# Kernel optimization log

Measured on AMD Instinct MI355X. Metric: run time of the kernel, lower is better.

Reference implementation:

```python
import jax, jax.numpy as jnp
import numpy as np

BN_EPS = 1e-5
RES_SCALE = 0.7


def setup_inputs() -> dict:
    key = jax.random.key(0)
    ks = jax.random.split(key, 10)
    N, IN_DIM, HID, E, L = 50000, 2000, 64, 1600000, 4
    features = jax.random.normal(ks[0], (N, IN_DIM), dtype=jnp.float32)
    edges = jax.random.randint(ks[1], (2, E), 0, N, dtype=jnp.int64)
    # GCNConv params: layer 0 is in_dim->hid, layers 1..3 are hid->hid
    W0 = jax.random.normal(ks[2], (IN_DIM, HID), dtype=jnp.float32) / np.sqrt(IN_DIM)
    b0 = jnp.zeros((HID,), dtype=jnp.float32)
    Wh = jax.random.normal(ks[3], (L - 1, HID, HID), dtype=jnp.float32) / np.sqrt(HID)
    bh = jnp.zeros((L - 1, HID), dtype=jnp.float32)
    # BatchNorm1d affine params per layer
    gamma = jnp.ones((L, HID), dtype=jnp.float32)
    beta = jnp.zeros((L, HID), dtype=jnp.float32)
    # learned layer-mixing weights (torch.randn init)
    lw = jax.random.normal(ks[4], (L,), dtype=jnp.float32)
    return {"features": features, "edges": edges, "W0": W0, "b0": b0,
            "Wh": Wh, "bh": bh, "gamma": gamma, "beta": beta, "lw": lw}


def reference(features, edges, W0, b0, Wh, bh, gamma, beta, lw):
    n = features.shape[0]
    src, dst = edges[0], edges[1]
    # GCN symmetric normalization with self-loops, edge_weight=1
    deg = jnp.zeros((n,), features.dtype).at[dst].add(1.0) + 1.0  # +1 self loop
    dinv = jax.lax.rsqrt(deg)
    enorm = dinv[src] * dinv[dst]       # [E]
    snorm = dinv * dinv                 # [N], self-loop norm

    def gcn_conv(x, W, b):
        xw = x @ W                                            # [N, H]
        agg = jnp.zeros_like(xw).at[dst].add(xw[src] * enorm[:, None])
        agg = agg + xw * snorm[:, None]
        return agg + b

    def batchnorm(x, g, bt):
        m = x.mean(axis=0)
        v = x.var(axis=0)  # biased variance, as in BN training normalization
        return (x - m) * jax.lax.rsqrt(v + BN_EPS) * g + bt

    L = gamma.shape[0]
    Ws = [W0] + [Wh[i] for i in range(L - 1)]
    bs = [b0] + [bh[i] for i in range(L - 1)]

    layer_out = []
    x = features
    for i in range(L):
        x = gcn_conv(x, Ws[i], bs[i])
        x = jax.nn.relu(batchnorm(x, gamma[i], beta[i]))
        if i > 0:
            x = x + RES_SCALE * layer_out[i - 1]
        layer_out.append(x)

    w = jax.nn.softmax(lw)
    emb = layer_out[0] * w[0]
    for i in range(1, L):
        emb = emb + layer_out[i] * w[i]
    return emb
```

## Files before the change

### kernel.cpp

```cpp
#include <hip/hip_runtime.h>
#include <hip/hip_bf16.h>
#include <math.h>

#define BN_EPS 1e-5f
#define RES_SCALE 0.7f

typedef float f4 __attribute__((ext_vector_type(4)));
typedef short s8 __attribute__((ext_vector_type(8)));

__device__ inline short f2bf(float f) {
    __hip_bfloat16 h = __float2bfloat16(f);
    return *reinterpret_cast<short*>(&h);
}

__global__ __launch_bounds__(256) void k_zero(int* counts, int* cursor, float* stats, int N, int S) {
    int i = blockIdx.x * 256 + threadIdx.x;
    if (i < N) { counts[i] = 0; cursor[i] = 0; }
    if (i < S) stats[i] = 0.0f;
}

__global__ __launch_bounds__(256) void k_count(const int* __restrict__ edges, int E, int* __restrict__ counts) {
    int e = blockIdx.x * 256 + threadIdx.x;
    if (e < E) atomicAdd(&counts[edges[E + e]], 1);
}

__global__ __launch_bounds__(256) void k_dinv(const int* __restrict__ counts, float* __restrict__ dinv, int N) {
    int i = blockIdx.x * 256 + threadIdx.x;
    if (i < N) dinv[i] = rsqrtf((float)counts[i] + 1.0f);
}

__global__ __launch_bounds__(256) void k_scan1(const int* __restrict__ counts, int* __restrict__ bsum, int N) {
    __shared__ int sd[256];
    int t = threadIdx.x;
    int base = blockIdx.x * 1024 + t * 4;
    int s = 0;
    if (base + 3 < N) { int4 v = *(const int4*)(counts + base); s = v.x + v.y + v.z + v.w; }
    else { for (int j = 0; j < 4; ++j) if (base + j < N) s += counts[base + j]; }
    sd[t] = s; __syncthreads();
    for (int off = 128; off > 0; off >>= 1) { if (t < off) sd[t] += sd[t + off]; __syncthreads(); }
    if (t == 0) bsum[blockIdx.x] = sd[0];
}

__global__ void k_scan2(int* bsum, int B, int* rowstart, int N) {
    if (threadIdx.x == 0 && blockIdx.x == 0) {
        int run = 0;
        for (int b = 0; b < B; ++b) { int v = bsum[b]; bsum[b] = run; run += v; }
        rowstart[N] = run;
    }
}

__global__ __launch_bounds__(256) void k_scan3(const int* __restrict__ counts, const int* __restrict__ bsum,
                                               int* __restrict__ rowstart, int N) {
    __shared__ int sd[256];
    int t = threadIdx.x;
    int base = blockIdx.x * 1024 + t * 4;
    int v0 = 0, v1 = 0, v2 = 0, v3 = 0;
    if (base + 3 < N) { int4 v = *(const int4*)(counts + base); v0 = v.x; v1 = v.y; v2 = v.z; v3 = v.w; }
    else {
        if (base < N) v0 = counts[base];
        if (base + 1 < N) v1 = counts[base + 1];
        if (base + 2 < N) v2 = counts[base + 2];
        if (base + 3 < N) v3 = counts[base + 3];
    }
    int s = v0 + v1 + v2 + v3;
    sd[t] = s; __syncthreads();
    for (int off = 1; off < 256; off <<= 1) {
        int add = (t >= off) ? sd[t - off] : 0;
        __syncthreads();
        sd[t] += add;
        __syncthreads();
    }
    int excl = sd[t] - s + bsum[blockIdx.x];
    if (base < N)     rowstart[base]     = excl;
    if (base + 1 < N) rowstart[base + 1] = excl + v0;
    if (base + 2 < N) rowstart[base + 2] = excl + v0 + v1;
    if (base + 3 < N) rowstart[base + 3] = excl + v0 + v1 + v2;
}

__global__ __launch_bounds__(256) void k_scatter(const int* __restrict__ edges, int E,
                                                 const int* __restrict__ rowstart, int* __restrict__ cursor,
                                                 const float* __restrict__ dinv,
                                                 int* __restrict__ colA, float* __restrict__ ewA) {
    int e = blockIdx.x * 256 + threadIdx.x;
    if (e >= E) return;
    int s = edges[e], d = edges[E + e];
    int pos = rowstart[d] + atomicAdd(&cursor[d], 1);
    colA[pos] = s;
    ewA[pos] = dinv[s] * dinv[d];
}

__global__ __launch_bounds__(256) void k_wt(const float* __restrict__ W0, const float* __restrict__ Wh,
                                            short* __restrict__ WT0, short* __restrict__ WTh, int K0) {
    __shared__ short Ts[64][72];
    int b = blockIdx.x, t = threadIdx.x;
    int nk0 = (K0 + 63) >> 6;
    const float* W; short* dst; int K, kt;
    if (b < nk0) { W = W0; dst = WT0; K = K0; kt = b * 64; }
    else { int l = b - nk0; W = Wh + (size_t)l * 64 * 64; dst = WTh + (size_t)l * 64 * 64; K = 64; kt = 0; }
    #pragma unroll
    for (int i = 0; i < 16; ++i) {
        int idx = t + i * 256;
        int r = idx >> 6, c = idx & 63;
        int gk = kt + r;
        Ts[c][r] = (gk < K) ? f2bf(W[(size_t)gk * 64 + c]) : (short)0;
    }
    __syncthreads();
    #pragma unroll
    for (int i = 0; i < 16; ++i) {
        int idx = t + i * 256;
        int n = idx >> 6, r = idx & 63;
        int gk = kt + r;
        if (gk < K) dst[(size_t)n * K + gk] = Ts[n][r];
    }
}

__global__ __launch_bounds__(256) void k_mm(const float* __restrict__ X, const short* __restrict__ WT,
                                            __hip_bfloat16* __restrict__ Cb, int N, int K) {
    __shared__ float Xs[64][36];
    __shared__ short Ws[64][40];
    int t = threadIdx.x;
    int w = t >> 6, lane = t & 63;
    int m = lane & 15, kq = lane >> 4;
    int row0 = blockIdx.x * 64;

    int xr = t >> 3, xc = t & 7;
    int wn = t >> 2, wc = t & 3;

    f4 acc[4] = {};
    f4 px0, px1; int4 pw;

    {
        int gr0 = row0 + xr, gr1 = row0 + xr + 32, gk = xc * 4;
        px0 = (gr0 < N && gk < K) ? *(const f4*)(X + (size_t)gr0 * K + gk) : (f4){};
        px1 = (gr1 < N && gk < K) ? *(const f4*)(X + (size_t)gr1 * K + gk) : (f4){};
        int gkw = wc * 8;
        pw = (gkw < K) ? *(const int4*)(WT + (size_t)wn * K + gkw) : make_int4(0, 0, 0, 0);
    }

    for (int kt = 0; kt < K; kt += 32) {
        *(f4*)&Xs[xr][xc * 4] = px0;
        *(f4*)&Xs[xr + 32][xc * 4] = px1;
        *(int4*)&Ws[wn][wc * 8] = pw;
        __syncthreads();

        int kn = kt + 32;
        if (kn < K) {
            int gr0 = row0 + xr, gr1 = row0 + xr + 32, gk = kn + xc * 4;
            px0 = (gr0 < N && gk < K) ? *(const f4*)(X + (size_t)gr0 * K + gk) : (f4){};
            px1 = (gr1 < N && gk < K) ? *(const f4*)(X + (size_t)gr1 * K + gk) : (f4){};
            int gkw = kn + wc * 8;
            pw = (gkw < K) ? *(const int4*)(WT + (size_t)wn * K + gkw) : make_int4(0, 0, 0, 0);
        }

        f4 a0 = *(const f4*)&Xs[w * 16 + m][kq * 8];
        f4 a1 = *(const f4*)&Xs[w * 16 + m][kq * 8 + 4];
        s8 av;
        #pragma unroll
        for (int j = 0; j < 4; ++j) { av[j] = f2bf(a0[j]); av[j + 4] = f2bf(a1[j]); }
        #pragma unroll
        for (int ct = 0; ct < 4; ++ct) {
            s8 bv = *(const s8*)&Ws[ct * 16 + m][kq * 8];
            acc[ct] = __builtin_amdgcn_mfma_f32_16x16x32_bf16(av, bv, acc[ct], 0, 0, 0);
        }
        __syncthreads();
    }

    #pragma unroll
    for (int ct = 0; ct < 4; ++ct) {
        #pragma unroll
        for (int reg = 0; reg < 4; ++reg) {
            int gr = row0 + w * 16 + kq * 4 + reg;
            if (gr < N) Cb[(size_t)gr * 64 + ct * 16 + m] = __float2bfloat16(acc[ct][reg]);
        }
    }
}

__global__ __launch_bounds__(256) void k_gather(const __hip_bfloat16* __restrict__ xw, const int* __restrict__ colA,
                                                const float* __restrict__ ewA, const int* __restrict__ rowstart,
                                                const float* __restrict__ dinv, float* __restrict__ agg, int N) {
    int wave = (blockIdx.x * 256 + threadIdx.x) >> 6;
    int lane = threadIdx.x & 63;
    if (wave >= N) return;
    int r = wave;
    float di = dinv[r];
    float acc = __bfloat162float(xw[(size_t)r * 64 + lane]) * di * di;
    int b = rowstart[r], e = rowstart[r + 1];
    int i = b;
    for (; i + 3 < e; i += 4) {
        int s0 = colA[i], s1 = colA[i + 1], s2 = colA[i + 2], s3 = colA[i + 3];
        float w0 = ewA[i], w1 = ewA[i + 1], w2 = ewA[i + 2], w3 = ewA[i + 3];
        float x0 = __bfloat162float(xw[(size_t)s0 * 64 + lane]);
        float x1 = __bfloat162float(xw[(size_t)s1 * 64 + lane]);
        float x2 = __bfloat162float(xw[(size_t)s2 * 64 + lane]);
        float x3 = __bfloat162float(xw[(size_t)s3 * 64 + lane]);
        acc += x0 * w0 + x1 * w1 + x2 * w2 + x3 * w3;
    }
    for (; i < e; ++i) acc += __bfloat162float(xw[(size_t)colA[i] * 64 + lane]) * ewA[i];
    agg[(size_t)r * 64 + lane] = acc;
}

__global__ __launch_bounds__(256) void k_stats(const float* __restrict__ x, float* __restrict__ stats, int N) {
    int col = threadIdx.x & 63;
    int sub = threadIdx.x >> 6;
    float s = 0.f, s2 = 0.f;
    for (int r = blockIdx.x * 4 + sub; r < N; r += gridDim.x * 4) {
        float v = x[(size_t)r * 64 + col];
        s += v; s2 += v * v;
    }
    __shared__ float sd[2][4][64];
    sd[0][sub][col] = s; sd[1][sub][col] = s2;
    __syncthreads();
    if (sub == 0) {
        s  = sd[0][0][col] + sd[0][1][col] + sd[0][2][col] + sd[0][3][col];
        s2 = sd[1][0][col] + sd[1][1][col] + sd[1][2][col] + sd[1][3][col];
        atomicAdd(&stats[col], s);
        atomicAdd(&stats[64 + col], s2);
    }
}

__global__ __launch_bounds__(256) void k_elem(const float* __restrict__ agg, const float* __restrict__ stats,
                                              const float* __restrict__ gamma, const float* __restrict__ beta,
                                              const float* __restrict__ lw, const float* __restrict__ xprev,
                                              float* __restrict__ xcur, float* __restrict__ emb,
                                              int N, int layer, int L) {
    int i = blockIdx.x * 256 + threadIdx.x;
    if (i >= N * 64) return;
    int c = i & 63;
    float rN = 1.0f / (float)N;
    float mn = stats[c] * rN;
    float var = stats[64 + c] * rN - mn * mn;
    float inv = rsqrtf(var + BN_EPS);
    float v = (agg[i] - mn) * inv * gamma[c] + beta[c];
    v = fmaxf(v, 0.0f);
    if (layer > 0) v += RES_SCALE * xprev[i];
    xcur[i] = v;
    float mx = lw[0];
    for (int j = 1; j < L; ++j) mx = fmaxf(mx, lw[j]);
    float sum = 0.f, wl = 0.f;
    for (int j = 0; j < L; ++j) {
        float e = __expf(lw[j] - mx);
        sum += e;
        if (j == layer) wl = e;
    }
    wl /= sum;
    float prev = (layer == 0) ? 0.0f : emb[i];
    emb[i] = prev + wl * v;
}

extern "C" void kernel_launch(void* const* d_in, const int* in_sizes, int n_in,
                              void* d_out, int out_size, void* d_ws, size_t ws_size,
                              hipStream_t stream) {
    const float* features = (const float*)d_in[0];
    const int*   edges    = (const int*)d_in[1];
    const float* W0       = (const float*)d_in[2];
    const float* Wh       = (const float*)d_in[4];
    const float* gamma    = (const float*)d_in[6];
    const float* beta     = (const float*)d_in[7];
    const float* lw       = (const float*)d_in[8];

    const int HID    = in_sizes[3];
    const int IN_DIM = in_sizes[2] / HID;
    const int N      = in_sizes[0] / IN_DIM;
    const int E      = in_sizes[1] / 2;
    const int L      = in_sizes[8];
    float* out = (float*)d_out;

    char* ws = (char*)d_ws;
    auto alloc = [&](size_t bytes) { char* p = ws; ws += (bytes + 255) & ~(size_t)255; return p; };
    int*   counts   = (int*)alloc((size_t)N * 4);
    int*   cursor   = (int*)alloc((size_t)N * 4);
    int*   rowstart = (int*)alloc((size_t)(N + 1) * 4);
    int*   bsum     = (int*)alloc(256 * 4);
    float* dinv     = (float*)alloc((size_t)N * 4);
    float* stats    = (float*)alloc((size_t)L * 128 * 4);
    int*   colA     = (int*)alloc((size_t)E * 4);
    float* ewA      = (float*)alloc((size_t)E * 4);
    short* WT0      = (short*)alloc((size_t)HID * IN_DIM * 2);
    short* WTh      = (short*)alloc((size_t)(L - 1) * HID * HID * 2);
    __hip_bfloat16* xw = (__hip_bfloat16*)alloc((size_t)N * HID * 2);
    float* agg      = (float*)alloc((size_t)N * HID * 4);
    float* x0       = (float*)alloc((size_t)N * HID * 4);
    float* x1       = (float*)alloc((size_t)N * HID * 4);

    int S = L * 128;
    int zgrid = (max(N, S) + 255) / 256;
    k_zero<<<zgrid, 256, 0, stream>>>(counts, cursor, stats, N, S);

    int egrid = (E + 255) / 256;
    int ngrid = (N + 255) / 256;
    k_count<<<egrid, 256, 0, stream>>>(edges, E, counts);
    k_dinv<<<ngrid, 256, 0, stream>>>(counts, dinv, N);

    int B = (N + 1023) / 1024;
    k_scan1<<<B, 256, 0, stream>>>(counts, bsum, N);
    k_scan2<<<1, 64, 0, stream>>>(bsum, B, rowstart, N);
    k_scan3<<<B, 256, 0, stream>>>(counts, bsum, rowstart, N);
    k_scatter<<<egrid, 256, 0, stream>>>(edges, E, rowstart, cursor, dinv, colA, ewA);

    int nk0 = (IN_DIM + 63) / 64;
    k_wt<<<nk0 + (L - 1), 256, 0, stream>>>(W0, Wh, WT0, WTh, IN_DIM);

    int mmgrid = (N + 63) / 64;
    int ggrid  = (N + 3) / 4;
    int elgrid = ((size_t)N * HID + 255) / 256;

    const float* xc_prev = nullptr;
    for (int l = 0; l < L; ++l) {
        const float* Xin = (l == 0) ? features : xc_prev;
        int K = (l == 0) ? IN_DIM : HID;
        const short* WTl = (l == 0) ? WT0 : WTh + (size_t)(l - 1) * HID * HID;
        k_mm<<<mmgrid, 256, 0, stream>>>(Xin, WTl, xw, N, K);
        k_gather<<<ggrid, 256, 0, stream>>>(xw, colA, ewA, rowstart, dinv, agg, N);
        k_stats<<<256, 256, 0, stream>>>(agg, stats + l * 128, N);
        float* xcur = (l % 2 == 0) ? x0 : x1;
        const float* xprev = (l == 0) ? nullptr : ((l % 2 == 0) ? x1 : x0);
        k_elem<<<elgrid, 256, 0, stream>>>(agg, stats + l * 128, gamma + l * HID, beta + l * HID,
                                           lw, xprev, xcur, out, N, l, L);
        xc_prev = xcur;
    }
}
```

Measured before the change: 1.140 ms.

## Fold GCN normalization into matmul epilogue and drop per-edge weights

Each row of the xw output is pre-scaled by dinv[src] in the matmul epilogue, and the gathered sum is scaled by dinv[dst] once per row. This removes the per-edge weight array and its writes and reads. The gather also loads column indices cooperatively, one per lane, and broadcasts them with readlane, processing 8 neighbours per step to raise memory-level parallelism. Rounding to bf16 now happens after the dinv scaling, which changes numerics slightly.

```diff
diff --git a/kernel.cpp b/kernel.cpp
--- a/kernel.cpp
+++ b/kernel.cpp
@@ -11,6 +11,10 @@
 __device__ inline short f2bf(float f) {
     __hip_bfloat16 h = __float2bfloat16(f);
     return *reinterpret_cast<short*>(&h);
+}
+
+__device__ inline float bf2f(unsigned short u) {
+    return __uint_as_float((unsigned)u << 16);
 }
 
 __global__ __launch_bounds__(256) void k_zero(int* counts, int* cursor, float* stats, int N, int S) {
@@ -79,14 +83,12 @@
 
 __global__ __launch_bounds__(256) void k_scatter(const int* __restrict__ edges, int E,
                                                  const int* __restrict__ rowstart, int* __restrict__ cursor,
-                                                 const float* __restrict__ dinv,
-                                                 int* __restrict__ colA, float* __restrict__ ewA) {
+                                                 int* __restrict__ colA) {
     int e = blockIdx.x * 256 + threadIdx.x;
     if (e >= E) return;
     int s = edges[e], d = edges[E + e];
     int pos = rowstart[d] + atomicAdd(&cursor[d], 1);
     colA[pos] = s;
-    ewA[pos] = dinv[s] * dinv[d];
 }
 
 __global__ __launch_bounds__(256) void k_wt(const float* __restrict__ W0, const float* __restrict__ Wh,
@@ -115,6 +117,7 @@
 }
 
 __global__ __launch_bounds__(256) void k_mm(const float* __restrict__ X, const short* __restrict__ WT,
+                                            const float* __restrict__ dinv,
                                             __hip_bfloat16* __restrict__ Cb, int N, int K) {
     __shared__ float Xs[64][36];
     __shared__ short Ws[64][40];
@@ -166,37 +169,57 @@
     }
 
     #pragma unroll
-    for (int ct = 0; ct < 4; ++ct) {
-        #pragma unroll
-        for (int reg = 0; reg < 4; ++reg) {
-            int gr = row0 + w * 16 + kq * 4 + reg;
-            if (gr < N) Cb[(size_t)gr * 64 + ct * 16 + m] = __float2bfloat16(acc[ct][reg]);
+    for (int reg = 0; reg < 4; ++reg) {
+        int gr = row0 + w * 16 + kq * 4 + reg;
+        if (gr < N) {
+            float di = dinv[gr];
+            #pragma unroll
+            for (int ct = 0; ct < 4; ++ct)
+                Cb[(size_t)gr * 64 + ct * 16 + m] = __float2bfloat16(acc[ct][reg] * di);
         }
     }
 }
 
 __global__ __launch_bounds__(256) void k_gather(const __hip_bfloat16* __restrict__ xw, const int* __restrict__ colA,
-                                                const float* __restrict__ ewA, const int* __restrict__ rowstart,
+                                                const int* __restrict__ rowstart,
                                                 const float* __restrict__ dinv, float* __restrict__ agg, int N) {
     int wave = (blockIdx.x * 256 + threadIdx.x) >> 6;
     int lane = threadIdx.x & 63;
     if (wave >= N) return;
     int r = wave;
-    float di = dinv[r];
-    float acc = __bfloat162float(xw[(size_t)r * 64 + lane]) * di * di;
+    const unsigned short* xwu = (const unsigned short*)xw;
+    float acc = bf2f(xwu[(size_t)r * 64 + lane]);
     int b = rowstart[r], e = rowstart[r + 1];
-    int i = b;
-    for (; i + 3 < e; i += 4) {
-        int s0 = colA[i], s1 = colA[i + 1], s2 = colA[i + 2], s3 = colA[i + 3];
-        float w0 = ewA[i], w1 = ewA[i + 1], w2 = ewA[i + 2], w3 = ewA[i + 3];
-        float x0 = __bfloat162float(xw[(size_t)s0 * 64 + lane]);
-        float x1 = __bfloat162float(xw[(size_t)s1 * 64 + lane]);
-        float x2 = __bfloat162float(xw[(size_t)s2 * 64 + lane]);
-        float x3 = __bfloat162float(xw[(size_t)s3 * 64 + lane]);
-        acc += x0 * w0 + x1 * w1 + x2 * w2 + x3 * w3;
-    }
-    for (; i < e; ++i) acc += __bfloat162float(xw[(size_t)colA[i] * 64 + lane]) * ewA[i];
-    agg[(size_t)r * 64 + lane] = acc;
+    for (int base = b; base < e; base += 64) {
+        int idx = base + lane;
+        int c = (idx < e) ? colA[idx] : 0;
+        int cnt = min(64, e - base);
+        int j = 0;
+        for (; j + 7 < cnt; j += 8) {
+            int s0 = __builtin_amdgcn_readlane(c, j);
+            int s1 = __builtin_amdgcn_readlane(c, j + 1);
+            int s2 = __builtin_amdgcn_readlane(c, j + 2);
+            int s3 = __builtin_amdgcn_readlane(c, j + 3);
+            int s4 = __builtin_amdgcn_readlane(c, j + 4);
+            int s5 = __builtin_amdgcn_readlane(c, j + 5);
+            int s6 = __builtin_amdgcn_readlane(c, j + 6);
+            int s7 = __builtin_amdgcn_readlane(c, j + 7);
+            float v0 = bf2f(xwu[(size_t)s0 * 64 + lane]);
+            float v1 = bf2f(xwu[(size_t)s1 * 64 + lane]);
+            float v2 = bf2f(xwu[(size_t)s2 * 64 + lane]);
+            float v3 = bf2f(xwu[(size_t)s3 * 64 + lane]);
+            float v4 = bf2f(xwu[(size_t)s4 * 64 + lane]);
+            float v5 = bf2f(xwu[(size_t)s5 * 64 + lane]);
+            float v6 = bf2f(xwu[(size_t)s6 * 64 + lane]);
+            float v7 = bf2f(xwu[(size_t)s7 * 64 + lane]);
+            acc += ((v0 + v1) + (v2 + v3)) + ((v4 + v5) + (v6 + v7));
+        }
+        for (; j < cnt; ++j) {
+            int s = __builtin_amdgcn_readlane(c, j);
+            acc += bf2f(xwu[(size_t)s * 64 + lane]);
+        }
+    }
+    agg[(size_t)r * 64 + lane] = acc * dinv[r];
 }
 
 __global__ __launch_bounds__(256) void k_stats(const float* __restrict__ x, float* __restrict__ stats, int N) {
@@ -274,7 +297,6 @@
     float* dinv     = (float*)alloc((size_t)N * 4);
     float* stats    = (float*)alloc((size_t)L * 128 * 4);
     int*   colA     = (int*)alloc((size_t)E * 4);
-    float* ewA      = (float*)alloc((size_t)E * 4);
     short* WT0      = (short*)alloc((size_t)HID * IN_DIM * 2);
     short* WTh      = (short*)alloc((size_t)(L - 1) * HID * HID * 2);
     __hip_bfloat16* xw = (__hip_bfloat16*)alloc((size_t)N * HID * 2);
@@ -295,7 +317,7 @@
     k_scan1<<<B, 256, 0, stream>>>(counts, bsum, N);
     k_scan2<<<1, 64, 0, stream>>>(bsum, B, rowstart, N);
     k_scan3<<<B, 256, 0, stream>>>(counts, bsum, rowstart, N);
-    k_scatter<<<egrid, 256, 0, stream>>>(edges, E, rowstart, cursor, dinv, colA, ewA);
+    k_scatter<<<egrid, 256, 0, stream>>>(edges, E, rowstart, cursor, colA);
 
     int nk0 = (IN_DIM + 63) / 64;
     k_wt<<<nk0 + (L - 1), 256, 0, stream>>>(W0, Wh, WT0, WTh, IN_DIM);
@@ -309,8 +331,8 @@
         const float* Xin = (l == 0) ? features : xc_prev;
         int K = (l == 0) ? IN_DIM : HID;
         const short* WTl = (l == 0) ? WT0 : WTh + (size_t)(l - 1) * HID * HID;
-        k_mm<<<mmgrid, 256, 0, stream>>>(Xin, WTl, xw, N, K);
-        k_gather<<<ggrid, 256, 0, stream>>>(xw, colA, ewA, rowstart, dinv, agg, N);
+        k_mm<<<mmgrid, 256, 0, stream>>>(Xin, WTl, dinv, xw, N, K);
+        k_gather<<<ggrid, 256, 0, stream>>>(xw, colA, rowstart, dinv, agg, N);
         k_stats<<<256, 256, 0, stream>>>(agg, stats + l * 128, N);
         float* xcur = (l % 2 == 0) ? x0 : x1;
         const float* xprev = (l == 0) ? nullptr : ((l % 2 == 0) ? x1 : x0);
```

After: 1.053 ms. -7.7%, faster.
